# Performance work log

Measured on AMD Instinct MI355X. Metric: run time of the kernel, lower is better.

The kernel has to match this reference:

```python
import jax, jax.numpy as jnp
import numpy as np

H, W = 32, 32
DIM = 768
NUM_BLOCKS = 4
BLOCK = DIM // NUM_BLOCKS
SCALE = 0.02


def setup_inputs() -> dict:
    key = jax.random.key(0)
    k0, k1, k2, k3, k4 = jax.random.split(key, 5)
    B, N, C = 64, H * W, DIM
    x = jax.random.normal(k0, (B, N, C), dtype=jnp.float32)
    w1 = SCALE * jax.random.normal(k1, (2, NUM_BLOCKS, BLOCK, BLOCK), dtype=jnp.float32)
    b1 = SCALE * jax.random.normal(k2, (2, NUM_BLOCKS, BLOCK), dtype=jnp.float32)
    w2 = SCALE * jax.random.normal(k3, (2, NUM_BLOCKS, BLOCK, BLOCK), dtype=jnp.float32)
    b2 = SCALE * jax.random.normal(k4, (2, NUM_BLOCKS, BLOCK), dtype=jnp.float32)
    return {"x": x, "w1": w1, "b1": b1, "w2": w2, "b2": b2}


def _mul(inp, weights):
    # inp: [B, H, Wf, blocks, d], weights: [blocks, d, k]
    return jnp.einsum('...bd,bdk->...bk', inp, weights)


def reference(x, w1, b1, w2, b2):
    B, N, C = x.shape
    xg = x.reshape(B, H, W, C)
    xf = jnp.fft.rfft2(xg, axes=(1, 2), norm='ortho')  # [B, H, W//2+1, C] complex64
    xf = xf.reshape(B, xf.shape[1], xf.shape[2], NUM_BLOCKS, BLOCK)
    xr, xi = xf.real, xf.imag
    # layer 1: complex block-diagonal linear + ReLU
    r1 = jax.nn.relu(_mul(xr, w1[0]) - _mul(xi, w1[1]) + b1[0])
    i1 = jax.nn.relu(_mul(xr, w1[1]) + _mul(xi, w1[0]) + b1[1])
    # layer 2 (faithful to original: imag uses the already-updated real part)
    r2 = _mul(r1, w2[0]) - _mul(i1, w2[1]) + b2[0]
    i2 = _mul(r2, w2[1]) + _mul(i1, w2[0]) + b2[1]
    xc = (r2 + 1j * i2).reshape(B, r2.shape[1], r2.shape[2], C)
    out = jnp.fft.irfft2(xc, s=(H, W), axes=(1, 2), norm='ortho')
    return out.reshape(B, N, C) + jnp.zeros_like(x)  # bias is zeros (self.bias is None)
```

## Files before the change

### kernel.cpp

```cpp
#include <hip/hip_runtime.h>
#include <cstddef>
#include <cstdint>


typedef __attribute__((ext_vector_type(8))) short bf16x8;
typedef __attribute__((ext_vector_type(4))) float f32x4;

namespace {

constexpr int BATCH = 64;
constexpr int Hh    = 32;
constexpr int Ww    = 32;
constexpr int WF    = 17;
constexpr int CC    = 768;
constexpr int BLK   = 192;

constexpr size_t W_ELEMS  = 16u * 36864u;
constexpr size_t TW_ELEMS = 4u * 1024u;
constexpr size_t PW_ELEMS = W_ELEMS + TW_ELEMS;

constexpr int PLANE_U = 48 * 512;
constexpr size_t SPEC_ELEMS = (size_t)BATCH * WF * 2 * PLANE_U;

constexpr float C32[32] = {
   1.0000000000f,  0.9807852804f,  0.9238795325f,  0.8314696123f,
   0.7071067812f,  0.5555702330f,  0.3826834324f,  0.1950903220f,
   0.0000000000f, -0.1950903220f, -0.3826834324f, -0.5555702330f,
  -0.7071067812f, -0.8314696123f, -0.9238795325f, -0.9807852804f,
  -1.0000000000f, -0.9807852804f, -0.9238795325f, -0.8314696123f,
  -0.7071067812f, -0.5555702330f, -0.3826834324f, -0.1950903220f,
   0.0000000000f,  0.1950903220f,  0.3826834324f,  0.5555702330f,
   0.7071067812f,  0.8314696123f,  0.9238795325f,  0.9807852804f
};
constexpr float S32[32] = {
   0.0000000000f,  0.1950903220f,  0.3826834324f,  0.5555702330f,
   0.7071067812f,  0.8314696123f,  0.9238795325f,  0.9807852804f,
   1.0000000000f,  0.9807852804f,  0.9238795325f,  0.8314696123f,
   0.7071067812f,  0.5555702330f,  0.3826834324f,  0.1950903220f,
   0.0000000000f, -0.1950903220f, -0.3826834324f, -0.5555702330f,
  -0.7071067812f, -0.8314696123f, -0.9238795325f, -0.9807852804f,
  -1.0000000000f, -0.9807852804f, -0.9238795325f, -0.8314696123f,
  -0.7071067812f, -0.5555702330f, -0.3826834324f, -0.1950903220f
};

}

__device__ __forceinline__ ushort f2bf(float f) {
    union { float f; unsigned u; } v; v.f = f;
    const unsigned r = (v.u + 0x7FFFu + ((v.u >> 16) & 1u)) >> 16;
    return (ushort)r;
}
__device__ __forceinline__ float bf2f(ushort u) {
    union { unsigned u; float f; } v; v.u = ((unsigned)u) << 16;
    return v.f;
}
__device__ __forceinline__ bf16x8 neg8(bf16x8 a) {
    union { bf16x8 v; uint4 u; } t; t.v = a;
    t.u.x ^= 0x80008000u; t.u.y ^= 0x80008000u;
    t.u.z ^= 0x80008000u; t.u.w ^= 0x80008000u;
    return t.v;
}

__global__ __launch_bounds__(256) void k_pack(const float* __restrict__ w1,
                                              const float* __restrict__ w2,
                                              ushort* __restrict__ pw) {
    const unsigned idx = blockIdx.x * 256u + threadIdx.x;
    if (idx < W_ELEMS) {
        const unsigned mi = idx / 36864u;
        const unsigned r  = idx % 36864u;
        const unsigned kk = r / 6144u;
        const unsigned r2 = r % 6144u;
        const unsigned nf = r2 / 512u;
        const unsigned r3 = r2 % 512u;
        const unsigned lane = r3 / 8u;
        const unsigned i  = r3 % 8u;
        const unsigned d   = kk * 32u + (lane >> 4) * 8u + i;
        const unsigned col = nf * 16u + (lane & 15u);
        const unsigned which = mi >> 2, blk = mi & 3u;
        const float* src = (which < 2u)
            ? (w1 + (size_t)(which * 4u + blk) * BLK * BLK)
            : (w2 + (size_t)((which - 2u) * 4u + blk) * BLK * BLK);
        pw[idx] = f2bf(src[(size_t)d * BLK + col]);
    } else if (idx < PW_ELEMS) {
        const unsigned t = idx - (unsigned)W_ELEMS;
        const unsigned mat = t >> 10;
        const unsigned rr  = t & 1023u;
        const unsigned mf  = rr >> 9;
        const unsigned q   = rr & 511u;
        const unsigned lane = q >> 3, i = q & 7u;
        const unsigned row = mf * 16u + (lane & 15u);
        const unsigned col = (lane >> 4) * 8u + i;
        const unsigned ang = (row * col) & 31u;
        float v;
        if      (mat == 0u) v = C32[ang] * 0.03125f;
        else if (mat == 1u) v = S32[ang] * 0.03125f;
        else if (mat == 2u) v = C32[ang];
        else                v = S32[ang];
        pw[idx] = f2bf(v);
    }
}

__global__ __launch_bounds__(256) void k_rfft_w(const float* __restrict__ x,
                                                ushort* __restrict__ spec) {
    const int bid = blockIdx.x;
    const int cc = bid % 3;
    const int hp = (bid / 3) & 15;
    const int b  = bid / 48;
    const int c  = cc * 256 + threadIdx.x;

    uint pr[17], pi[17];
    const float* p0 = x + ((size_t)b * 1024 + hp * 64) * CC + c;
#pragma unroll
    for (int half = 0; half < 2; ++half) {
        const float* px = p0 + (size_t)half * 32 * CC;
        float v[32];
#pragma unroll
        for (int w = 0; w < 32; ++w) v[w] = px[(size_t)w * CC];
        float av[16], bv[16];
#pragma unroll
        for (int w = 1; w <= 15; ++w) { av[w] = v[w] + v[32 - w]; bv[w] = v[w] - v[32 - w]; }
#pragma unroll
        for (int k = 0; k <= 16; ++k) {
            float sr = v[0] + ((k & 1) ? -v[16] : v[16]);
            float si = 0.f;
#pragma unroll
            for (int w = 1; w <= 15; ++w) {
                const int t = (k * w) & 31;
                sr = fmaf(av[w],  C32[t], sr);
                si = fmaf(bv[w], -S32[t], si);
            }
            if (half == 0) { pr[k] = f2bf(sr); pi[k] = f2bf(si); }
            else { pr[k] |= (uint)f2bf(sr) << 16; pi[k] |= (uint)f2bf(si) << 16; }
        }
    }
    const size_t base = (size_t)b * (WF * 2 * PLANE_U)
                      + (size_t)(c >> 4) * 512 + hp * 32
                      + (((c & 15) ^ ((hp & 7) << 1)) << 1);
#pragma unroll
    for (int k = 0; k <= 16; ++k) {
        *(uint*)(spec + base + (size_t)k * (2 * PLANE_U)) = pr[k];
        *(uint*)(spec + base + (size_t)k * (2 * PLANE_U) + PLANE_U) = pi[k];
    }
}

__global__ __launch_bounds__(256, 3) void k_fft_mix(
        ushort* __restrict__ spec,
        const ushort* __restrict__ pw,
        const float* __restrict__ b1, const float* __restrict__ b2) {

    __shared__ ushort lds[4][6336];

    const int bid = blockIdx.x;
    const int blk = bid / (BATCH * WF);
    const int rem = bid % (BATCH * WF);
    const int b   = rem / WF;
    const int kw  = rem % WF;
    const int tid = threadIdx.x;
    const int wv = tid >> 6, l = tid & 63, lc = l & 15, lg = l >> 4;

    const size_t gR = ((size_t)(b * WF + kw) * 2) * PLANE_U + blk * 6144;
    const size_t gI = gR + PLANE_U;

#pragma unroll
    for (int j = 0; j < 3; ++j) {
        const int q = tid + 256 * j;
        const int dst = (q >> 6) * 528 + (q & 63) * 8;
        *(uint4*)&lds[0][dst] = *(const uint4*)(spec + gR + q * 8);
        *(uint4*)&lds[1][dst] = *(const uint4*)(spec + gI + q * 8);
    }
    __syncthreads();

    const ushort* TW = pw + W_ELEMS;
    const int col0 = wv * 48;

    {
        bf16x8 xr[3], xi[3];
#pragma unroll
        for (int n = 0; n < 3; ++n) {
            const int csub = wv * 3 + n;
            union { bf16x8 v; uint d[4]; } ur, ui;
#pragma unroll
            for (int t = 0; t < 4; ++t) {
                const int hp = lg * 4 + t;
                const int pos = csub * 528 + hp * 32 + ((lc ^ ((hp & 7) << 1)) << 1);
                ur.d[t] = *(const uint*)&lds[0][pos];
                ui.d[t] = *(const uint*)&lds[1][pos];
            }
            xr[n] = ur.v; xi[n] = ui.v;
        }
        bf16x8 cf[2], sf[2], sfn[2];
#pragma unroll
        for (int m = 0; m < 2; ++m) {
            cf[m]  = *(const bf16x8*)(TW + ((size_t)(0 * 2 + m) * 64 + l) * 8);
            sf[m]  = *(const bf16x8*)(TW + ((size_t)(1 * 2 + m) * 64 + l) * 8);
            sfn[m] = neg8(sf[m]);
        }
        f32x4 yr[2][3] = {}, yi[2][3] = {};
#pragma unroll
        for (int m = 0; m < 2; ++m)
#pragma unroll
            for (int n = 0; n < 3; ++n) {
                yr[m][n] = __builtin_amdgcn_mfma_f32_16x16x32_bf16(cf[m],  xr[n], yr[m][n], 0, 0, 0);
                yr[m][n] = __builtin_amdgcn_mfma_f32_16x16x32_bf16(sf[m],  xi[n], yr[m][n], 0, 0, 0);
                yi[m][n] = __builtin_amdgcn_mfma_f32_16x16x32_bf16(cf[m],  xi[n], yi[m][n], 0, 0, 0);
                yi[m][n] = __builtin_amdgcn_mfma_f32_16x16x32_bf16(sfn[m], xr[n], yi[m][n], 0, 0, 0);
            }
#pragma unroll
        for (int m = 0; m < 2; ++m)
#pragma unroll
            for (int n = 0; n < 3; ++n)
#pragma unroll
                for (int r = 0; r < 4; ++r) {
                    const int pos = (wv * 3 + n) * 528 + (m * 16 + lg * 4 + r) * 16 + lc;
                    lds[0][pos] = f2bf(yr[m][n][r]);
                    lds[1][pos] = f2bf(yi[m][n][r]);
                }
    }
    __syncthreads();

    const ushort* pW1r = pw + (size_t)(0 * 4 + blk) * 36864;
    const ushort* pW1i = pw + (size_t)(1 * 4 + blk) * 36864;
    const ushort* pW2r = pw + (size_t)(2 * 4 + blk) * 36864;
    const ushort* pW2i = pw + (size_t)(3 * 4 + blk) * 36864;

    {
        f32x4 aR[2][3], aI[2][3];
#pragma unroll
        for (int n = 0; n < 3; ++n) {
            const float br = b1[(size_t)(0 * 4 + blk) * BLK + col0 + n * 16 + lc];
            const float bi = b1[(size_t)(1 * 4 + blk) * BLK + col0 + n * 16 + lc];
#pragma unroll
            for (int m = 0; m < 2; ++m) {
                aR[m][n] = (f32x4){br, br, br, br};
                aI[m][n] = (f32x4){bi, bi, bi, bi};
            }
        }
#pragma unroll
        for (int kk = 0; kk < 6; ++kk) {
            const int csubA = 2 * kk + (lg >> 1);
            const int apos  = csubA * 528 + lc * 16 + (lg & 1) * 8;
            bf16x8 ar[2], ai[2], ain[2];
#pragma unroll
            for (int m = 0; m < 2; ++m) {
                ar[m]  = *(const bf16x8*)&lds[0][apos + m * 256];
                ai[m]  = *(const bf16x8*)&lds[1][apos + m * 256];
                ain[m] = neg8(ai[m]);
            }
            bf16x8 wr[3], wi[3];
#pragma unroll
            for (int n = 0; n < 3; ++n) {
                const size_t off = ((size_t)(kk * 12 + wv * 3 + n) * 64 + l) * 8;
                wr[n] = *(const bf16x8*)(pW1r + off);
                wi[n] = *(const bf16x8*)(pW1i + off);
            }
#pragma unroll
            for (int m = 0; m < 2; ++m)
#pragma unroll
                for (int n = 0; n < 3; ++n) {
                    aR[m][n] = __builtin_amdgcn_mfma_f32_16x16x32_bf16(ar[m],  wr[n], aR[m][n], 0, 0, 0);
                    aR[m][n] = __builtin_amdgcn_mfma_f32_16x16x32_bf16(ain[m], wi[n], aR[m][n], 0, 0, 0);
                    aI[m][n] = __builtin_amdgcn_mfma_f32_16x16x32_bf16(ar[m],  wi[n], aI[m][n], 0, 0, 0);
                    aI[m][n] = __builtin_amdgcn_mfma_f32_16x16x32_bf16(ai[m],  wr[n], aI[m][n], 0, 0, 0);
                }
        }
        __syncthreads();
#pragma unroll
        for (int m = 0; m < 2; ++m)
#pragma unroll
            for (int n = 0; n < 3; ++n)
#pragma unroll
                for (int r = 0; r < 4; ++r) {
                    float rv = aR[m][n][r]; rv = rv > 0.f ? rv : 0.f;
                    float iv = aI[m][n][r]; iv = iv > 0.f ? iv : 0.f;
                    const int pos = (wv * 3 + n) * 528 + (m * 16 + lg * 4 + r) * 16 + lc;
                    lds[2][pos] = f2bf(rv);
                    lds[3][pos] = f2bf(iv);
                }
    }
    __syncthreads();

    {
        f32x4 cR[2][3];
#pragma unroll
        for (int n = 0; n < 3; ++n) {
            const float br = b2[(size_t)(0 * 4 + blk) * BLK + col0 + n * 16 + lc];
#pragma unroll
            for (int m = 0; m < 2; ++m) cR[m][n] = (f32x4){br, br, br, br};
        }
#pragma unroll
        for (int kk = 0; kk < 6; ++kk) {
            const int csubA = 2 * kk + (lg >> 1);
            const int apos  = csubA * 528 + lc * 16 + (lg & 1) * 8;
            bf16x8 ar[2], ain[2];
#pragma unroll
            for (int m = 0; m < 2; ++m) {
                ar[m]  = *(const bf16x8*)&lds[2][apos + m * 256];
                ain[m] = neg8(*(const bf16x8*)&lds[3][apos + m * 256]);
            }
            bf16x8 wr[3], wi[3];
#pragma unroll
            for (int n = 0; n < 3; ++n) {
                const size_t off = ((size_t)(kk * 12 + wv * 3 + n) * 64 + l) * 8;
                wr[n] = *(const bf16x8*)(pW2r + off);
                wi[n] = *(const bf16x8*)(pW2i + off);
            }
#pragma unroll
            for (int m = 0; m < 2; ++m)
#pragma unroll
                for (int n = 0; n < 3; ++n) {
                    cR[m][n] = __builtin_amdgcn_mfma_f32_16x16x32_bf16(ar[m],  wr[n], cR[m][n], 0, 0, 0);
                    cR[m][n] = __builtin_amdgcn_mfma_f32_16x16x32_bf16(ain[m], wi[n], cR[m][n], 0, 0, 0);
                }
        }
#pragma unroll
        for (int m = 0; m < 2; ++m)
#pragma unroll
            for (int n = 0; n < 3; ++n) {
                const int csub = wv * 3 + n;
#pragma unroll
                for (int rp = 0; rp < 2; ++rp) {
                    const ushort lo = f2bf(cR[m][n][2 * rp]);
                    const ushort hi = f2bf(cR[m][n][2 * rp + 1]);
                    const int kh0 = m * 16 + lg * 4 + 2 * rp;
                    lds[0][csub * 528 + kh0 * 16 + lc]       = lo;
                    lds[0][csub * 528 + (kh0 + 1) * 16 + lc] = hi;
                    const int hp = kh0 >> 1;
                    const int post = csub * 528 + hp * 32 + ((lc ^ ((hp & 7) << 1)) << 1);
                    *(uint*)&lds[1][post] = (uint)lo | ((uint)hi << 16);
                }
            }
    }
    __syncthreads();

    f32x4 cI[2][3];
    {
#pragma unroll
        for (int n = 0; n < 3; ++n) {
            const float bi = b2[(size_t)(1 * 4 + blk) * BLK + col0 + n * 16 + lc];
#pragma unroll
            for (int m = 0; m < 2; ++m) cI[m][n] = (f32x4){bi, bi, bi, bi};
        }
#pragma unroll
        for (int kk = 0; kk < 6; ++kk) {
            const int csubA = 2 * kk + (lg >> 1);
            const int apos  = csubA * 528 + lc * 16 + (lg & 1) * 8;
            bf16x8 a2[2], i1[2];
#pragma unroll
            for (int m = 0; m < 2; ++m) {
                a2[m] = *(const bf16x8*)&lds[0][apos + m * 256];
                i1[m] = *(const bf16x8*)&lds[3][apos + m * 256];
            }
            bf16x8 wr[3], wi[3];
#pragma unroll
            for (int n = 0; n < 3; ++n) {
                const size_t off = ((size_t)(kk * 12 + wv * 3 + n) * 64 + l) * 8;
                wr[n] = *(const bf16x8*)(pW2r + off);
                wi[n] = *(const bf16x8*)(pW2i + off);
            }
#pragma unroll
            for (int m = 0; m < 2; ++m)
#pragma unroll
                for (int n = 0; n < 3; ++n) {
                    cI[m][n] = __builtin_amdgcn_mfma_f32_16x16x32_bf16(a2[m], wi[n], cI[m][n], 0, 0, 0);
                    cI[m][n] = __builtin_amdgcn_mfma_f32_16x16x32_bf16(i1[m], wr[n], cI[m][n], 0, 0, 0);
                }
        }
#pragma unroll
        for (int m = 0; m < 2; ++m)
#pragma unroll
            for (int n = 0; n < 3; ++n) {
                const int csub = wv * 3 + n;
#pragma unroll
                for (int rp = 0; rp < 2; ++rp) {
                    const int hp = (m * 16 + lg * 4 + 2 * rp) >> 1;
                    const int post = csub * 528 + hp * 32 + ((lc ^ ((hp & 7) << 1)) << 1);
                    *(uint*)&lds[2][post] =
                        (uint)f2bf(cI[m][n][2 * rp]) | ((uint)f2bf(cI[m][n][2 * rp + 1]) << 16);
                }
            }
    }

    {
        bf16x8 ci[2], si[2], sin_[2];
#pragma unroll
        for (int m = 0; m < 2; ++m) {
            ci[m]   = *(const bf16x8*)(TW + ((size_t)(2 * 2 + m) * 64 + l) * 8);
            si[m]   = *(const bf16x8*)(TW + ((size_t)(3 * 2 + m) * 64 + l) * 8);
            sin_[m] = neg8(si[m]);
        }
        bf16x8 r2b[3], i2b[3];
#pragma unroll
        for (int n = 0; n < 3; ++n) {
            const int csub = wv * 3 + n;
            union { bf16x8 v; uint d[4]; } ur, ui;
#pragma unroll
            for (int t = 0; t < 4; ++t) {
                const int hp = lg * 4 + t;
                const int pos = csub * 528 + hp * 32 + ((lc ^ ((hp & 7) << 1)) << 1);
                ur.d[t] = *(const uint*)&lds[1][pos];
                ui.d[t] = *(const uint*)&lds[2][pos];
            }
            r2b[n] = ur.v; i2b[n] = ui.v;
        }
        f32x4 zr[2][3] = {}, zi[2][3] = {};
#pragma unroll
        for (int m = 0; m < 2; ++m)
#pragma unroll
            for (int n = 0; n < 3; ++n) {
                zr[m][n] = __builtin_amdgcn_mfma_f32_16x16x32_bf16(ci[m],   r2b[n], zr[m][n], 0, 0, 0);
                zr[m][n] = __builtin_amdgcn_mfma_f32_16x16x32_bf16(sin_[m], i2b[n], zr[m][n], 0, 0, 0);
                zi[m][n] = __builtin_amdgcn_mfma_f32_16x16x32_bf16(ci[m],   i2b[n], zi[m][n], 0, 0, 0);
                zi[m][n] = __builtin_amdgcn_mfma_f32_16x16x32_bf16(si[m],   r2b[n], zi[m][n], 0, 0, 0);
            }
#pragma unroll
        for (int m = 0; m < 2; ++m)
#pragma unroll
            for (int n = 0; n < 3; ++n) {
                const size_t cbase = gR + (size_t)(wv * 3 + n) * 512;
#pragma unroll
                for (int rp = 0; rp < 2; ++rp) {
                    const int hp = (m * 16 + lg * 4 + 2 * rp) >> 1;
                    const size_t pos = cbase + hp * 32 + ((lc ^ ((hp & 7) << 1)) << 1);
                    *(uint*)(spec + pos) =
                        (uint)f2bf(zr[m][n][2 * rp]) | ((uint)f2bf(zr[m][n][2 * rp + 1]) << 16);
                    *(uint*)(spec + pos + PLANE_U) =
                        (uint)f2bf(zi[m][n][2 * rp]) | ((uint)f2bf(zi[m][n][2 * rp + 1]) << 16);
                }
            }
    }
}

__global__ __launch_bounds__(256) void k_irfft_w(const ushort* __restrict__ spec,
                                                 float* __restrict__ out) {
    const int bid = blockIdx.x;
    const int cc = bid % 3;
    const int hp = (bid / 3) & 15;
    const int b  = bid / 48;
    const int c  = cc * 256 + threadIdx.x;

    const size_t base = (size_t)b * (WF * 2 * PLANE_U)
                      + (size_t)(c >> 4) * 512 + hp * 32
                      + (((c & 15) ^ ((hp & 7) << 1)) << 1);
    float xr0[17], xi0[17], xr1[17], xi1[17];
#pragma unroll
    for (int k = 0; k <= 16; ++k) {
        const uint ur = *(const uint*)(spec + base + (size_t)k * (2 * PLANE_U));
        const uint ui = *(const uint*)(spec + base + (size_t)k * (2 * PLANE_U) + PLANE_U);
        xr0[k] = bf2f((ushort)ur); xr1[k] = bf2f((ushort)(ur >> 16));
        xi0[k] = bf2f((ushort)ui); xi1[k] = bf2f((ushort)(ui >> 16));
    }
    float* po0 = out + ((size_t)b * 1024 + hp * 64) * CC + c;
    float* po1 = po0 + (size_t)32 * CC;
#pragma unroll
    for (int w = 0; w <= 16; ++w) {
        float e0 = xr0[0] + ((w & 1) ? -xr0[16] : xr0[16]);
        float e1 = xr1[0] + ((w & 1) ? -xr1[16] : xr1[16]);
        float o0 = 0.f, o1 = 0.f;
#pragma unroll
        for (int k = 1; k <= 15; ++k) {
            const int t = (k * w) & 31;
            e0 = fmaf(2.f * xr0[k],  C32[t], e0);
            o0 = fmaf(2.f * xi0[k], -S32[t], o0);
            e1 = fmaf(2.f * xr1[k],  C32[t], e1);
            o1 = fmaf(2.f * xi1[k], -S32[t], o1);
        }
        po0[(size_t)w * CC] = (e0 + o0) * 0.03125f;
        po1[(size_t)w * CC] = (e1 + o1) * 0.03125f;
        if (w >= 1 && w <= 15) {
            po0[(size_t)(32 - w) * CC] = (e0 - o0) * 0.03125f;
            po1[(size_t)(32 - w) * CC] = (e1 - o1) * 0.03125f;
        }
    }
}

extern "C" void kernel_launch(void* const* d_in, const int* in_sizes, int n_in,
                              void* d_out, int out_size, void* d_ws, size_t ws_size,
                              hipStream_t stream) {
    const float* x  = (const float*)d_in[0];
    const float* w1 = (const float*)d_in[1];
    const float* b1 = (const float*)d_in[2];
    const float* w2 = (const float*)d_in[3];
    const float* b2 = (const float*)d_in[4];
    float* out = (float*)d_out;

    ushort* pw   = (ushort*)d_ws;
    ushort* spec = pw + PW_ELEMS;

    k_pack<<<dim3((unsigned)((PW_ELEMS + 255) / 256)), dim3(256), 0, stream>>>(w1, w2, pw);
    k_rfft_w<<<dim3(BATCH * 16 * 3), dim3(256), 0, stream>>>(x, spec);
    k_fft_mix<<<dim3(4 * BATCH * WF), dim3(256), 0, stream>>>(spec, pw, b1, b2);
    k_irfft_w<<<dim3(BATCH * 16 * 3), dim3(256), 0, stream>>>(spec, out);
}
```

Before: 253.2 us.

## Move W-axis rfft/irfft to MFMA DFT matmuls and pre-negate packed weights

The scalar FMA-based W-dimension real FFT and inverse FFT kernels are replaced with bf16 MFMA matrix multiplies against precomputed DFT twiddle matrices. Input tiles are staged through LDS with swizzled layouts, and blocks are re-split into four channel quarters. The pack kernel now also emits negated weight and twiddle matrices, so the mix kernel drops its in-register sign flips at the cost of extra weight loads. This aims to cut ALU-bound FFT time, but adds bf16 rounding inside the DFT stages and uses more LDS per block.

```diff
diff --git a/kernel.cpp b/kernel.cpp
--- a/kernel.cpp
+++ b/kernel.cpp
@@ -9,18 +9,15 @@
 namespace {
 
 constexpr int BATCH = 64;
-constexpr int Hh    = 32;
-constexpr int Ww    = 32;
 constexpr int WF    = 17;
 constexpr int CC    = 768;
 constexpr int BLK   = 192;
 
-constexpr size_t W_ELEMS  = 16u * 36864u;
-constexpr size_t TW_ELEMS = 4u * 1024u;
+constexpr size_t W_ELEMS  = 24u * 36864u;
+constexpr size_t TW_ELEMS = 8u * 1024u;
 constexpr size_t PW_ELEMS = W_ELEMS + TW_ELEMS;
 
 constexpr int PLANE_U = 48 * 512;
-constexpr size_t SPEC_ELEMS = (size_t)BATCH * WF * 2 * PLANE_U;
 
 constexpr float C32[32] = {
    1.0000000000f,  0.9807852804f,  0.9238795325f,  0.8314696123f,
@@ -50,15 +47,8 @@
     const unsigned r = (v.u + 0x7FFFu + ((v.u >> 16) & 1u)) >> 16;
     return (ushort)r;
 }
-__device__ __forceinline__ float bf2f(ushort u) {
-    union { unsigned u; float f; } v; v.u = ((unsigned)u) << 16;
-    return v.f;
-}
-__device__ __forceinline__ bf16x8 neg8(bf16x8 a) {
-    union { bf16x8 v; uint4 u; } t; t.v = a;
-    t.u.x ^= 0x80008000u; t.u.y ^= 0x80008000u;
-    t.u.z ^= 0x80008000u; t.u.w ^= 0x80008000u;
-    return t.v;
+__device__ __forceinline__ uint pk(float lo, float hi) {
+    return (uint)f2bf(lo) | ((uint)f2bf(hi) << 16);
 }
 
 __global__ __launch_bounds__(256) void k_pack(const float* __restrict__ w1,
@@ -76,11 +66,15 @@
         const unsigned i  = r3 % 8u;
         const unsigned d   = kk * 32u + (lane >> 4) * 8u + i;
         const unsigned col = nf * 16u + (lane & 15u);
-        const unsigned which = mi >> 2, blk = mi & 3u;
-        const float* src = (which < 2u)
-            ? (w1 + (size_t)(which * 4u + blk) * BLK * BLK)
-            : (w2 + (size_t)((which - 2u) * 4u + blk) * BLK * BLK);
-        pw[idx] = f2bf(src[(size_t)d * BLK + col]);
+        const unsigned mat = mi >> 2, blk = mi & 3u;
+        const float* src; float sgn = 1.f;
+        if      (mat == 0u) src = w1 + (size_t)(0 * 4 + blk) * BLK * BLK;
+        else if (mat == 1u) src = w1 + (size_t)(1 * 4 + blk) * BLK * BLK;
+        else if (mat == 2u) { src = w1 + (size_t)(1 * 4 + blk) * BLK * BLK; sgn = -1.f; }
+        else if (mat == 3u) src = w2 + (size_t)(0 * 4 + blk) * BLK * BLK;
+        else if (mat == 4u) src = w2 + (size_t)(1 * 4 + blk) * BLK * BLK;
+        else                { src = w2 + (size_t)(1 * 4 + blk) * BLK * BLK; sgn = -1.f; }
+        pw[idx] = f2bf(sgn * src[(size_t)d * BLK + col]);
     } else if (idx < PW_ELEMS) {
         const unsigned t = idx - (unsigned)W_ELEMS;
         const unsigned mat = t >> 10;
@@ -94,53 +88,94 @@
         float v;
         if      (mat == 0u) v = C32[ang] * 0.03125f;
         else if (mat == 1u) v = S32[ang] * 0.03125f;
-        else if (mat == 2u) v = C32[ang];
-        else                v = S32[ang];
+        else if (mat == 2u) v = -S32[ang] * 0.03125f;
+        else if (mat == 3u) v = C32[ang];
+        else if (mat == 4u) v = S32[ang];
+        else if (mat == 5u) v = -S32[ang];
+        else if (mat == 6u) {
+            if      (col == 0u)  v = 0.03125f;
+            else if (col < 16u)  v = 2.f * C32[ang] * 0.03125f;
+            else if (col == 16u) v = C32[(16u * row) & 31u] * 0.03125f;
+            else                 v = 0.f;
+        } else {
+            v = (col >= 1u && col <= 15u) ? (-2.f * S32[ang] * 0.03125f) : 0.f;
+        }
         pw[idx] = f2bf(v);
     }
 }
 
 __global__ __launch_bounds__(256) void k_rfft_w(const float* __restrict__ x,
-                                                ushort* __restrict__ spec) {
+                                                ushort* __restrict__ spec,
+                                                const ushort* __restrict__ pw) {
+    __shared__ uint xb[16 * 384];
+
     const int bid = blockIdx.x;
-    const int cc = bid % 3;
-    const int hp = (bid / 3) & 15;
-    const int b  = bid / 48;
-    const int c  = cc * 256 + threadIdx.x;
-
-    uint pr[17], pi[17];
-    const float* p0 = x + ((size_t)b * 1024 + hp * 64) * CC + c;
-#pragma unroll
-    for (int half = 0; half < 2; ++half) {
-        const float* px = p0 + (size_t)half * 32 * CC;
-        float v[32];
-#pragma unroll
-        for (int w = 0; w < 32; ++w) v[w] = px[(size_t)w * CC];
-        float av[16], bv[16];
-#pragma unroll
-        for (int w = 1; w <= 15; ++w) { av[w] = v[w] + v[32 - w]; bv[w] = v[w] - v[32 - w]; }
-#pragma unroll
-        for (int k = 0; k <= 16; ++k) {
-            float sr = v[0] + ((k & 1) ? -v[16] : v[16]);
-            float si = 0.f;
-#pragma unroll
-            for (int w = 1; w <= 15; ++w) {
-                const int t = (k * w) & 31;
-                sr = fmaf(av[w],  C32[t], sr);
-                si = fmaf(bv[w], -S32[t], si);
-            }
-            if (half == 0) { pr[k] = f2bf(sr); pi[k] = f2bf(si); }
-            else { pr[k] |= (uint)f2bf(sr) << 16; pi[k] |= (uint)f2bf(si) << 16; }
-        }
-    }
-    const size_t base = (size_t)b * (WF * 2 * PLANE_U)
-                      + (size_t)(c >> 4) * 512 + hp * 32
-                      + (((c & 15) ^ ((hp & 7) << 1)) << 1);
-#pragma unroll
-    for (int k = 0; k <= 16; ++k) {
-        *(uint*)(spec + base + (size_t)k * (2 * PLANE_U)) = pr[k];
-        *(uint*)(spec + base + (size_t)k * (2 * PLANE_U) + PLANE_U) = pi[k];
-    }
+    const int cq = bid & 3;
+    const int hp = (bid >> 2) & 15;
+    const int b  = bid >> 6;
+    const int tid = threadIdx.x;
+    const int wv = tid >> 6, l = tid & 63, lc = l & 15, lg = l >> 4;
+
+#pragma unroll
+    for (int it = 0; it < 6; ++it) {
+        const int flat = it * 256 + tid;
+        const int h  = flat / 768;
+        const int rm = flat % 768;
+        const int wp = rm / 48;
+        const int c4 = rm % 48;
+        const float* p = x + ((size_t)(b * 1024 + (hp * 2 + h) * 32 + wp * 2) * CC)
+                           + cq * 192 + c4 * 4;
+        const float4 a  = *(const float4*)p;
+        const float4 bb = *(const float4*)(p + CC);
+        uint4 u;
+        u.x = pk(a.x, bb.x); u.y = pk(a.y, bb.y);
+        u.z = pk(a.z, bb.z); u.w = pk(a.w, bb.w);
+        const int col = (h * 192 + c4 * 4) ^ (((wp >> 2) & 3) << 3);
+        *(uint4*)&xb[wp * 384 + col] = u;
+    }
+    __syncthreads();
+
+    const ushort* TW = pw + W_ELEMS;
+    bf16x8 ac[2], as[2];
+#pragma unroll
+    for (int m = 0; m < 2; ++m) {
+        ac[m] = *(const bf16x8*)(TW + ((size_t)(3 * 2 + m) * 64 + l) * 8);
+        as[m] = *(const bf16x8*)(TW + ((size_t)(5 * 2 + m) * 64 + l) * 8);
+    }
+
+    f32x4 aR[2][6] = {}, aI[2][6] = {};
+#pragma unroll
+    for (int j = 0; j < 6; ++j) {
+        const int nf = (j < 3) ? (wv * 3 + j) : (12 + wv * 3 + (j - 3));
+        union { bf16x8 v; uint d[4]; } u;
+#pragma unroll
+        for (int t = 0; t < 4; ++t) {
+            const int wp = lg * 4 + t;
+            u.d[t] = xb[wp * 384 + ((nf * 16 + lc) ^ (lg << 3))];
+        }
+#pragma unroll
+        for (int m = 0; m < 2; ++m) {
+            aR[m][j] = __builtin_amdgcn_mfma_f32_16x16x32_bf16(ac[m], u.v, aR[m][j], 0, 0, 0);
+            aI[m][j] = __builtin_amdgcn_mfma_f32_16x16x32_bf16(as[m], u.v, aI[m][j], 0, 0, 0);
+        }
+    }
+
+    uint* spec32 = (uint*)spec;
+    const int swz = (hp & 7) << 1;
+#pragma unroll
+    for (int m = 0; m < 2; ++m)
+#pragma unroll
+        for (int j = 0; j < 3; ++j)
+#pragma unroll
+            for (int r = 0; r < 4; ++r) {
+                if (m == 1 && (lg != 0 || r != 0)) continue;
+                const int kw = m * 16 + lg * 4 + r;
+                const int csub = cq * 12 + wv * 3 + j;
+                const size_t pos = ((size_t)(b * WF + kw) * 2) * 12288
+                                 + csub * 256 + hp * 16 + (lc ^ swz);
+                spec32[pos]         = pk(aR[m][j][r], aR[m][j + 3][r]);
+                spec32[pos + 12288] = pk(aI[m][j][r], aI[m][j + 3][r]);
+            }
 }
 
 __global__ __launch_bounds__(256, 3) void k_fft_mix(
@@ -193,7 +228,7 @@
         for (int m = 0; m < 2; ++m) {
             cf[m]  = *(const bf16x8*)(TW + ((size_t)(0 * 2 + m) * 64 + l) * 8);
             sf[m]  = *(const bf16x8*)(TW + ((size_t)(1 * 2 + m) * 64 + l) * 8);
-            sfn[m] = neg8(sf[m]);
+            sfn[m] = *(const bf16x8*)(TW + ((size_t)(2 * 2 + m) * 64 + l) * 8);
         }
         f32x4 yr[2][3] = {}, yi[2][3] = {};
 #pragma unroll
@@ -210,18 +245,22 @@
 #pragma unroll
             for (int n = 0; n < 3; ++n)
 #pragma unroll
-                for (int r = 0; r < 4; ++r) {
-                    const int pos = (wv * 3 + n) * 528 + (m * 16 + lg * 4 + r) * 16 + lc;
-                    lds[0][pos] = f2bf(yr[m][n][r]);
-                    lds[1][pos] = f2bf(yi[m][n][r]);
+                for (int rp = 0; rp < 2; ++rp) {
+                    const uint ur = pk(yr[m][n][2 * rp], yr[m][n][2 * rp + 1]);
+                    const uint ui = pk(yi[m][n][2 * rp], yi[m][n][2 * rp + 1]);
+                    const int p0 = (wv * 3 + n) * 528 + (m * 16 + lg * 4 + 2 * rp) * 16 + lc;
+                    lds[0][p0] = (ushort)ur; lds[0][p0 + 16] = (ushort)(ur >> 16);
+                    lds[1][p0] = (ushort)ui; lds[1][p0 + 16] = (ushort)(ui >> 16);
                 }
     }
     __syncthreads();
 
-    const ushort* pW1r = pw + (size_t)(0 * 4 + blk) * 36864;
-    const ushort* pW1i = pw + (size_t)(1 * 4 + blk) * 36864;
-    const ushort* pW2r = pw + (size_t)(2 * 4 + blk) * 36864;
-    const ushort* pW2i = pw + (size_t)(3 * 4 + blk) * 36864;
+    const ushort* pW1r  = pw + (size_t)(0 * 4 + blk) * 36864;
+    const ushort* pW1i  = pw + (size_t)(1 * 4 + blk) * 36864;
+    const ushort* pW1in = pw + (size_t)(2 * 4 + blk) * 36864;
+    const ushort* pW2r  = pw + (size_t)(3 * 4 + blk) * 36864;
+    const ushort* pW2i  = pw + (size_t)(4 * 4 + blk) * 36864;
+    const ushort* pW2in = pw + (size_t)(5 * 4 + blk) * 36864;
 
     {
         f32x4 aR[2][3], aI[2][3];
@@ -239,28 +278,28 @@
         for (int kk = 0; kk < 6; ++kk) {
             const int csubA = 2 * kk + (lg >> 1);
             const int apos  = csubA * 528 + lc * 16 + (lg & 1) * 8;
-            bf16x8 ar[2], ai[2], ain[2];
+            bf16x8 ar[2], ai[2];
 #pragma unroll
             for (int m = 0; m < 2; ++m) {
-                ar[m]  = *(const bf16x8*)&lds[0][apos + m * 256];
-                ai[m]  = *(const bf16x8*)&lds[1][apos + m * 256];
-                ain[m] = neg8(ai[m]);
-            }
-            bf16x8 wr[3], wi[3];
+                ar[m] = *(const bf16x8*)&lds[0][apos + m * 256];
+                ai[m] = *(const bf16x8*)&lds[1][apos + m * 256];
+            }
+            bf16x8 wr[3], wi[3], wn[3];
 #pragma unroll
             for (int n = 0; n < 3; ++n) {
                 const size_t off = ((size_t)(kk * 12 + wv * 3 + n) * 64 + l) * 8;
                 wr[n] = *(const bf16x8*)(pW1r + off);
                 wi[n] = *(const bf16x8*)(pW1i + off);
+                wn[n] = *(const bf16x8*)(pW1in + off);
             }
 #pragma unroll
             for (int m = 0; m < 2; ++m)
 #pragma unroll
                 for (int n = 0; n < 3; ++n) {
-                    aR[m][n] = __builtin_amdgcn_mfma_f32_16x16x32_bf16(ar[m],  wr[n], aR[m][n], 0, 0, 0);
-                    aR[m][n] = __builtin_amdgcn_mfma_f32_16x16x32_bf16(ain[m], wi[n], aR[m][n], 0, 0, 0);
-                    aI[m][n] = __builtin_amdgcn_mfma_f32_16x16x32_bf16(ar[m],  wi[n], aI[m][n], 0, 0, 0);
-                    aI[m][n] = __builtin_amdgcn_mfma_f32_16x16x32_bf16(ai[m],  wr[n], aI[m][n], 0, 0, 0);
+                    aR[m][n] = __builtin_amdgcn_mfma_f32_16x16x32_bf16(ar[m], wr[n], aR[m][n], 0, 0, 0);
+                    aR[m][n] = __builtin_amdgcn_mfma_f32_16x16x32_bf16(ai[m], wn[n], aR[m][n], 0, 0, 0);
+                    aI[m][n] = __builtin_amdgcn_mfma_f32_16x16x32_bf16(ar[m], wi[n], aI[m][n], 0, 0, 0);
+                    aI[m][n] = __builtin_amdgcn_mfma_f32_16x16x32_bf16(ai[m], wr[n], aI[m][n], 0, 0, 0);
                 }
         }
         __syncthreads();
@@ -269,12 +308,12 @@
 #pragma unroll
             for (int n = 0; n < 3; ++n)
 #pragma unroll
-                for (int r = 0; r < 4; ++r) {
-                    float rv = aR[m][n][r]; rv = rv > 0.f ? rv : 0.f;
-                    float iv = aI[m][n][r]; iv = iv > 0.f ? iv : 0.f;
-                    const int pos = (wv * 3 + n) * 528 + (m * 16 + lg * 4 + r) * 16 + lc;
-                    lds[2][pos] = f2bf(rv);
-                    lds[3][pos] = f2bf(iv);
+                for (int rp = 0; rp < 2; ++rp) {
+                    const uint ur = pk(fmaxf(aR[m][n][2 * rp], 0.f), fmaxf(aR[m][n][2 * rp + 1], 0.f));
+                    const uint ui = pk(fmaxf(aI[m][n][2 * rp], 0.f), fmaxf(aI[m][n][2 * rp + 1], 0.f));
+                    const int p0 = (wv * 3 + n) * 528 + (m * 16 + lg * 4 + 2 * rp) * 16 + lc;
+                    lds[2][p0] = (ushort)ur; lds[2][p0 + 16] = (ushort)(ur >> 16);
+                    lds[3][p0] = (ushort)ui; lds[3][p0 + 16] = (ushort)(ui >> 16);
                 }
     }
     __syncthreads();
@@ -291,25 +330,25 @@
         for (int kk = 0; kk < 6; ++kk) {
             const int csubA = 2 * kk + (lg >> 1);
             const int apos  = csubA * 528 + lc * 16 + (lg & 1) * 8;
-            bf16x8 ar[2], ain[2];
+            bf16x8 ar[2], ii[2];
 #pragma unroll
             for (int m = 0; m < 2; ++m) {
-                ar[m]  = *(const bf16x8*)&lds[2][apos + m * 256];
-                ain[m] = neg8(*(const bf16x8*)&lds[3][apos + m * 256]);
-            }
-            bf16x8 wr[3], wi[3];
+                ar[m] = *(const bf16x8*)&lds[2][apos + m * 256];
+                ii[m] = *(const bf16x8*)&lds[3][apos + m * 256];
+            }
+            bf16x8 wr[3], wn[3];
 #pragma unroll
             for (int n = 0; n < 3; ++n) {
                 const size_t off = ((size_t)(kk * 12 + wv * 3 + n) * 64 + l) * 8;
                 wr[n] = *(const bf16x8*)(pW2r + off);
-                wi[n] = *(const bf16x8*)(pW2i + off);
+                wn[n] = *(const bf16x8*)(pW2in + off);
             }
 #pragma unroll
             for (int m = 0; m < 2; ++m)
 #pragma unroll
                 for (int n = 0; n < 3; ++n) {
-                    cR[m][n] = __builtin_amdgcn_mfma_f32_16x16x32_bf16(ar[m],  wr[n], cR[m][n], 0, 0, 0);
-                    cR[m][n] = __builtin_amdgcn_mfma_f32_16x16x32_bf16(ain[m], wi[n], cR[m][n], 0, 0, 0);
+                    cR[m][n] = __builtin_amdgcn_mfma_f32_16x16x32_bf16(ar[m], wr[n], cR[m][n], 0, 0, 0);
+                    cR[m][n] = __builtin_amdgcn_mfma_f32_16x16x32_bf16(ii[m], wn[n], cR[m][n], 0, 0, 0);
                 }
         }
 #pragma unroll
@@ -319,21 +358,20 @@
                 const int csub = wv * 3 + n;
 #pragma unroll
                 for (int rp = 0; rp < 2; ++rp) {
-                    const ushort lo = f2bf(cR[m][n][2 * rp]);
-                    const ushort hi = f2bf(cR[m][n][2 * rp + 1]);
+                    const uint p = pk(cR[m][n][2 * rp], cR[m][n][2 * rp + 1]);
                     const int kh0 = m * 16 + lg * 4 + 2 * rp;
-                    lds[0][csub * 528 + kh0 * 16 + lc]       = lo;
-                    lds[0][csub * 528 + (kh0 + 1) * 16 + lc] = hi;
+                    lds[0][csub * 528 + kh0 * 16 + lc]       = (ushort)p;
+                    lds[0][csub * 528 + (kh0 + 1) * 16 + lc] = (ushort)(p >> 16);
                     const int hp = kh0 >> 1;
                     const int post = csub * 528 + hp * 32 + ((lc ^ ((hp & 7) << 1)) << 1);
-                    *(uint*)&lds[1][post] = (uint)lo | ((uint)hi << 16);
+                    *(uint*)&lds[1][post] = p;
                 }
             }
     }
     __syncthreads();
 
-    f32x4 cI[2][3];
     {
+        f32x4 cI[2][3];
 #pragma unroll
         for (int n = 0; n < 3; ++n) {
             const float bi = b2[(size_t)(1 * 4 + blk) * BLK + col0 + n * 16 + lc];
@@ -350,12 +388,12 @@
                 a2[m] = *(const bf16x8*)&lds[0][apos + m * 256];
                 i1[m] = *(const bf16x8*)&lds[3][apos + m * 256];
             }
-            bf16x8 wr[3], wi[3];
+            bf16x8 wi[3], wr[3];
 #pragma unroll
             for (int n = 0; n < 3; ++n) {
                 const size_t off = ((size_t)(kk * 12 + wv * 3 + n) * 64 + l) * 8;
+                wi[n] = *(const bf16x8*)(pW2i + off);
                 wr[n] = *(const bf16x8*)(pW2r + off);
-                wi[n] = *(const bf16x8*)(pW2i + off);
             }
 #pragma unroll
             for (int m = 0; m < 2; ++m)
@@ -374,19 +412,18 @@
                 for (int rp = 0; rp < 2; ++rp) {
                     const int hp = (m * 16 + lg * 4 + 2 * rp) >> 1;
                     const int post = csub * 528 + hp * 32 + ((lc ^ ((hp & 7) << 1)) << 1);
-                    *(uint*)&lds[2][post] =
-                        (uint)f2bf(cI[m][n][2 * rp]) | ((uint)f2bf(cI[m][n][2 * rp + 1]) << 16);
+                    *(uint*)&lds[2][post] = pk(cI[m][n][2 * rp], cI[m][n][2 * rp + 1]);
                 }
             }
     }
 
     {
-        bf16x8 ci[2], si[2], sin_[2];
+        bf16x8 ci[2], si[2], sn[2];
 #pragma unroll
         for (int m = 0; m < 2; ++m) {
-            ci[m]   = *(const bf16x8*)(TW + ((size_t)(2 * 2 + m) * 64 + l) * 8);
-            si[m]   = *(const bf16x8*)(TW + ((size_t)(3 * 2 + m) * 64 + l) * 8);
-            sin_[m] = neg8(si[m]);
+            ci[m] = *(const bf16x8*)(TW + ((size_t)(3 * 2 + m) * 64 + l) * 8);
+            si[m] = *(const bf16x8*)(TW + ((size_t)(4 * 2 + m) * 64 + l) * 8);
+            sn[m] = *(const bf16x8*)(TW + ((size_t)(5 * 2 + m) * 64 + l) * 8);
         }
         bf16x8 r2b[3], i2b[3];
 #pragma unroll
@@ -407,10 +444,10 @@
         for (int m = 0; m < 2; ++m)
 #pragma unroll
             for (int n = 0; n < 3; ++n) {
-                zr[m][n] = __builtin_amdgcn_mfma_f32_16x16x32_bf16(ci[m],   r2b[n], zr[m][n], 0, 0, 0);
-                zr[m][n] = __builtin_amdgcn_mfma_f32_16x16x32_bf16(sin_[m], i2b[n], zr[m][n], 0, 0, 0);
-                zi[m][n] = __builtin_amdgcn_mfma_f32_16x16x32_bf16(ci[m],   i2b[n], zi[m][n], 0, 0, 0);
-                zi[m][n] = __builtin_amdgcn_mfma_f32_16x16x32_bf16(si[m],   r2b[n], zi[m][n], 0, 0, 0);
+                zr[m][n] = __builtin_amdgcn_mfma_f32_16x16x32_bf16(ci[m], r2b[n], zr[m][n], 0, 0, 0);
+                zr[m][n] = __builtin_amdgcn_mfma_f32_16x16x32_bf16(sn[m], i2b[n], zr[m][n], 0, 0, 0);
+                zi[m][n] = __builtin_amdgcn_mfma_f32_16x16x32_bf16(ci[m], i2b[n], zi[m][n], 0, 0, 0);
+                zi[m][n] = __builtin_amdgcn_mfma_f32_16x16x32_bf16(si[m], r2b[n], zi[m][n], 0, 0, 0);
             }
 #pragma unroll
         for (int m = 0; m < 2; ++m)
@@ -421,56 +458,99 @@
                 for (int rp = 0; rp < 2; ++rp) {
                     const int hp = (m * 16 + lg * 4 + 2 * rp) >> 1;
                     const size_t pos = cbase + hp * 32 + ((lc ^ ((hp & 7) << 1)) << 1);
-                    *(uint*)(spec + pos) =
-                        (uint)f2bf(zr[m][n][2 * rp]) | ((uint)f2bf(zr[m][n][2 * rp + 1]) << 16);
-                    *(uint*)(spec + pos + PLANE_U) =
-                        (uint)f2bf(zi[m][n][2 * rp]) | ((uint)f2bf(zi[m][n][2 * rp + 1]) << 16);
+                    *(uint*)(spec + pos)           = pk(zr[m][n][2 * rp], zr[m][n][2 * rp + 1]);
+                    *(uint*)(spec + pos + PLANE_U) = pk(zi[m][n][2 * rp], zi[m][n][2 * rp + 1]);
                 }
             }
     }
 }
 
 __global__ __launch_bounds__(256) void k_irfft_w(const ushort* __restrict__ spec,
-                                                 float* __restrict__ out) {
+                                                 float* __restrict__ out,
+                                                 const ushort* __restrict__ pw) {
+    __shared__ uint rawR[17 * 198];
+    __shared__ uint rawI[17 * 198];
+
     const int bid = blockIdx.x;
-    const int cc = bid % 3;
-    const int hp = (bid / 3) & 15;
-    const int b  = bid / 48;
-    const int c  = cc * 256 + threadIdx.x;
-
-    const size_t base = (size_t)b * (WF * 2 * PLANE_U)
-                      + (size_t)(c >> 4) * 512 + hp * 32
-                      + (((c & 15) ^ ((hp & 7) << 1)) << 1);
-    float xr0[17], xi0[17], xr1[17], xi1[17];
-#pragma unroll
-    for (int k = 0; k <= 16; ++k) {
-        const uint ur = *(const uint*)(spec + base + (size_t)k * (2 * PLANE_U));
-        const uint ui = *(const uint*)(spec + base + (size_t)k * (2 * PLANE_U) + PLANE_U);
-        xr0[k] = bf2f((ushort)ur); xr1[k] = bf2f((ushort)(ur >> 16));
-        xi0[k] = bf2f((ushort)ui); xi1[k] = bf2f((ushort)(ui >> 16));
-    }
-    float* po0 = out + ((size_t)b * 1024 + hp * 64) * CC + c;
-    float* po1 = po0 + (size_t)32 * CC;
-#pragma unroll
-    for (int w = 0; w <= 16; ++w) {
-        float e0 = xr0[0] + ((w & 1) ? -xr0[16] : xr0[16]);
-        float e1 = xr1[0] + ((w & 1) ? -xr1[16] : xr1[16]);
-        float o0 = 0.f, o1 = 0.f;
-#pragma unroll
-        for (int k = 1; k <= 15; ++k) {
-            const int t = (k * w) & 31;
-            e0 = fmaf(2.f * xr0[k],  C32[t], e0);
-            o0 = fmaf(2.f * xi0[k], -S32[t], o0);
-            e1 = fmaf(2.f * xr1[k],  C32[t], e1);
-            o1 = fmaf(2.f * xi1[k], -S32[t], o1);
-        }
-        po0[(size_t)w * CC] = (e0 + o0) * 0.03125f;
-        po1[(size_t)w * CC] = (e1 + o1) * 0.03125f;
-        if (w >= 1 && w <= 15) {
-            po0[(size_t)(32 - w) * CC] = (e0 - o0) * 0.03125f;
-            po1[(size_t)(32 - w) * CC] = (e1 - o1) * 0.03125f;
-        }
-    }
+    const int cq = bid & 3;
+    const int hp = (bid >> 2) & 15;
+    const int b  = bid >> 6;
+    const int tid = threadIdx.x;
+    const int wv = tid >> 6, l = tid & 63, lc = l & 15, lg = l >> 4;
+
+    const uint* spec32 = (const uint*)spec;
+
+#pragma unroll
+    for (int it = 0; it < 13; ++it) {
+        const int slot = it * 256 + tid;
+        if (slot < 3264) {
+            const int part = slot & 7;
+            const int c2   = slot >> 3;
+            const int plane = c2 / 204;
+            const int q  = c2 % 204;
+            const int kw = q / 12, csub = q % 12;
+            const size_t gpos = ((size_t)(b * WF + kw) * 2 + plane) * 12288
+                              + (cq * 12 + csub) * 256 + hp * 16 + part * 2;
+            const uint2 v = *(const uint2*)(spec32 + gpos);
+            uint* dst = plane ? rawI : rawR;
+            *(uint2*)&dst[kw * 198 + csub * 16 + part * 2] = v;
+        }
+    }
+    __syncthreads();
+
+    const ushort* TW = pw + W_ELEMS;
+    bf16x8 twA[2], twB[2];
+#pragma unroll
+    for (int m = 0; m < 2; ++m) {
+        twA[m] = *(const bf16x8*)(TW + ((size_t)(6 * 2 + m) * 64 + l) * 8);
+        twB[m] = *(const bf16x8*)(TW + ((size_t)(7 * 2 + m) * 64 + l) * 8);
+    }
+
+    int rowoff[8];
+#pragma unroll
+    for (int i = 0; i < 8; ++i) {
+        int kwv = lg * 8 + i;
+        if (kwv > 16) kwv = 16;
+        rowoff[i] = kwv * 396;
+    }
+
+    const ushort* rr = (const ushort*)rawR;
+    const ushort* ri = (const ushort*)rawI;
+    const int swz = (hp & 7) << 1;
+
+    f32x4 acc[2][6] = {};
+#pragma unroll
+    for (int j = 0; j < 6; ++j) {
+        const int coll = (wv * 6 + j) * 16 + lc;
+        const int h  = coll & 1;
+        const int cL = coll >> 1;
+        const int bu = ((cL >> 4) * 16 + ((cL & 15) ^ swz)) * 2 + h;
+        union { bf16x8 v; ushort s[8]; } fr, fi;
+#pragma unroll
+        for (int i = 0; i < 8; ++i) {
+            fr.s[i] = rr[rowoff[i] + bu];
+            fi.s[i] = ri[rowoff[i] + bu];
+        }
+#pragma unroll
+        for (int m = 0; m < 2; ++m) {
+            acc[m][j] = __builtin_amdgcn_mfma_f32_16x16x32_bf16(twA[m], fr.v, acc[m][j], 0, 0, 0);
+            acc[m][j] = __builtin_amdgcn_mfma_f32_16x16x32_bf16(twB[m], fi.v, acc[m][j], 0, 0, 0);
+        }
+    }
+
+#pragma unroll
+    for (int m = 0; m < 2; ++m)
+#pragma unroll
+        for (int j = 0; j < 6; ++j) {
+            const int coll = (wv * 6 + j) * 16 + lc;
+            const int h  = coll & 1;
+            const int c  = cq * 192 + (coll >> 1);
+#pragma unroll
+            for (int r = 0; r < 4; ++r) {
+                const int w = m * 16 + lg * 4 + r;
+                out[((size_t)(b * 1024 + (hp * 2 + h) * 32 + w)) * CC + c] = acc[m][j][r];
+            }
+        }
 }
 
 extern "C" void kernel_launch(void* const* d_in, const int* in_sizes, int n_in,
@@ -486,8 +566,8 @@
     ushort* pw   = (ushort*)d_ws;
     ushort* spec = pw + PW_ELEMS;
 
-    k_pack<<<dim3((unsigned)((PW_ELEMS + 255) / 256)), dim3(256), 0, stream>>>(w1, w2, pw);
-    k_rfft_w<<<dim3(BATCH * 16 * 3), dim3(256), 0, stream>>>(x, spec);
+    k_pack<<<dim3((unsigned)(PW_ELEMS / 256)), dim3(256), 0, stream>>>(w1, w2, pw);
+    k_rfft_w<<<dim3(BATCH * 16 * 4), dim3(256), 0, stream>>>(x, spec, pw);
     k_fft_mix<<<dim3(4 * BATCH * WF), dim3(256), 0, stream>>>(spec, pw, b1, b2);
-    k_irfft_w<<<dim3(BATCH * 16 * 3), dim3(256), 0, stream>>>(spec, out);
-}
+    k_irfft_w<<<dim3(BATCH * 16 * 4), dim3(256), 0, stream>>>(spec, out, pw);
+}
```

New measurement: 263.8 us. 1.04x slower.
